# Kernel optimization log

Hardware: AMD Instinct MI355X
Metric: run time of the kernel (lower is better)

Reference implementation:

```python
import jax, jax.numpy as jnp
import numpy as np

B, N, C, D, K, H = 32, 4096, 128, 64, 8, 128  # batch, tokens, in_dim, slot_dim, num_slots, mlp hidden
SCALE = D ** -0.5
EPS = 1e-8
ITERS = 3


def _ln(x, g, b):
    m = jnp.mean(x, axis=-1, keepdims=True)
    v = jnp.var(x, axis=-1, keepdims=True)
    return (x - m) * jax.lax.rsqrt(v + 1e-5) * g + b


def _gru(x, h, wih, whh, bih, bhh):
    # torch.nn.GRUCell semantics; x:[M,D], h:[M,D], wih/whh:[3D,D]
    gi = x @ wih.T + bih
    gh = h @ whh.T + bhh
    i_r, i_z, i_n = jnp.split(gi, 3, axis=-1)
    h_r, h_z, h_n = jnp.split(gh, 3, axis=-1)
    r = jax.nn.sigmoid(i_r + h_r)
    z = jax.nn.sigmoid(i_z + h_z)
    n = jnp.tanh(i_n + r * h_n)
    return (1.0 - z) * n + z * h


def setup_inputs() -> dict:
    key = jax.random.key(0)
    ks = jax.random.split(key, 24)
    f32 = jnp.float32

    def rn(i, shape, scale):
        return (jax.random.normal(ks[i], shape, f32) * scale)

    return {
        "feat": jax.random.normal(ks[0], (B, N, C), f32),
        "slot": jax.random.normal(ks[1], (B, K, D), f32),
        "norm_feat_g": jnp.ones((C,), f32), "norm_feat_b": jnp.zeros((C,), f32),
        "Wk": rn(2, (C, D), C ** -0.5), "Wv": rn(3, (C, D), C ** -0.5),
        "q_ln_g": jnp.ones((D,), f32), "q_ln_b": jnp.zeros((D,), f32),
        "Wq": rn(4, (D, D), D ** -0.5),
        "qbg_ln_g": jnp.ones((D,), f32), "qbg_ln_b": jnp.zeros((D,), f32),
        "Wq_bg": rn(5, (D, D), D ** -0.5),
        "gru_wih": rn(6, (3 * D, D), D ** -0.5), "gru_whh": rn(7, (3 * D, D), D ** -0.5),
        "gru_bih": jnp.zeros((3 * D,), f32), "gru_bhh": jnp.zeros((3 * D,), f32),
        "grubg_wih": rn(8, (3 * D, D), D ** -0.5), "grubg_whh": rn(9, (3 * D, D), D ** -0.5),
        "grubg_bih": jnp.zeros((3 * D,), f32), "grubg_bhh": jnp.zeros((3 * D,), f32),
        "res_ln_g": jnp.ones((D,), f32), "res_ln_b": jnp.zeros((D,), f32),
        "res_w1": rn(10, (D, H), D ** -0.5), "res_b1": jnp.zeros((H,), f32),
        "res_w2": rn(11, (H, D), H ** -0.5), "res_b2": jnp.zeros((D,), f32),
        "resbg_ln_g": jnp.ones((D,), f32), "resbg_ln_b": jnp.zeros((D,), f32),
        "resbg_w1": rn(12, (D, H), D ** -0.5), "resbg_b1": jnp.zeros((H,), f32),
        "resbg_w2": rn(13, (H, D), H ** -0.5), "resbg_b2": jnp.zeros((D,), f32),
    }


def reference(feat, slot, norm_feat_g, norm_feat_b, Wk, Wv,
              q_ln_g, q_ln_b, Wq, qbg_ln_g, qbg_ln_b, Wq_bg,
              gru_wih, gru_whh, gru_bih, gru_bhh,
              grubg_wih, grubg_whh, grubg_bih, grubg_bhh,
              res_ln_g, res_ln_b, res_w1, res_b1, res_w2, res_b2,
              resbg_ln_g, resbg_ln_b, resbg_w1, resbg_b1, resbg_w2, resbg_b2):
    # split externally-provided slots (slot is not None branch)
    slot_bg = slot[:, :1, :]   # [B,1,D]   (bg_slot_dim == fg_slot_dim == D)
    slot_fg = slot[:, 1:, :]   # [B,K-1,D]

    x = _ln(feat, norm_feat_g, norm_feat_b)   # [B,N,C]
    k = x @ Wk                                 # [B,N,D]
    v = x @ Wv                                 # [B,N,D]

    attn = None
    for _ in range(ITERS):
        q_fg = _ln(slot_fg, q_ln_g, q_ln_b) @ Wq          # [B,K-1,D]
        q_bg = _ln(slot_bg, qbg_ln_g, qbg_ln_b) @ Wq_bg   # [B,1,D]
        dots_fg = jnp.einsum('bid,bjd->bij', q_fg, k) * SCALE
        dots_bg = jnp.einsum('bid,bjd->bij', q_bg, k) * SCALE
        dots = jnp.concatenate([dots_bg, dots_fg], axis=1)  # [B,K,N]
        attn = jax.nn.softmax(dots, axis=1) + EPS            # softmax over slots
        attn_bg, attn_fg = attn[:, :1, :], attn[:, 1:, :]
        w_bg = attn_bg / jnp.sum(attn_bg, axis=-1, keepdims=True)
        w_fg = attn_fg / jnp.sum(attn_fg, axis=-1, keepdims=True)
        upd_fg = jnp.einsum('bjd,bij->bid', v, w_fg)  # [B,K-1,D]
        upd_bg = jnp.einsum('bjd,bij->bid', v, w_bg)  # [B,1,D]

        s_bg = _gru(upd_bg.reshape(-1, D), slot_bg.reshape(-1, D),
                    grubg_wih, grubg_whh, grubg_bih, grubg_bhh).reshape(B, 1, D)
        slot_bg = s_bg + (jax.nn.relu(_ln(s_bg, resbg_ln_g, resbg_ln_b) @ resbg_w1 + resbg_b1) @ resbg_w2 + resbg_b2)

        s_fg = _gru(upd_fg.reshape(-1, D), slot_fg.reshape(-1, D),
                    gru_wih, gru_whh, gru_bih, gru_bhh).reshape(B, K - 1, D)
        slot_fg = s_fg + (jax.nn.relu(_ln(s_fg, res_ln_g, res_ln_b) @ res_w1 + res_b1) @ res_w2 + res_b2)

    slots = jnp.concatenate([slot_bg, slot_fg], axis=1)  # [B,K,D]
    return slots, attn
```

## Files before the change

### kernel.cpp

```cpp
#include <hip/hip_runtime.h>
#include <hip/hip_bf16.h>

constexpr int BB = 32;
constexpr int NN = 4096;
constexpr int CC = 128;
constexpr int DD = 64;
constexpr int KK = 8;
constexpr int HH = 128;
constexpr float SCALE = 0.125f;
constexpr float EPS_A = 1e-8f;
constexpr float LN_EPS = 1e-5f;

constexpr int NTIL = 64;

typedef __bf16 bfx8 __attribute__((ext_vector_type(8)));
typedef float f32x4 __attribute__((ext_vector_type(4)));

__device__ inline float wave_sum(float x) {
#pragma unroll
    for (int off = 32; off > 0; off >>= 1) x += __shfl_xor(x, off, 64);
    return x;
}

__device__ inline float lane_bcast(float v, int src) {
    return __uint_as_float(__builtin_amdgcn_readlane(__float_as_uint(v), src));
}

__device__ inline float sigmoidf_(float x) { return 1.f / (1.f + __expf(-x)); }

__device__ inline unsigned short bf16rne(float x) {
    unsigned u = __float_as_uint(x);
    unsigned r = u + 0x7fffu + ((u >> 16) & 1u);
    return (unsigned short)(r >> 16);
}
__device__ inline float bf16tof(unsigned short h) {
    return __uint_as_float(((unsigned)h) << 16);
}

__global__ __launch_bounds__(256) void k0_prepw(
    const float* __restrict__ Wk, const float* __restrict__ Wv,
    unsigned short* __restrict__ fragW)
{
    const int o = blockIdx.x * 256 + threadIdx.x;
    const int j = o & 7, l = (o >> 3) & 63, nf = (o >> 9) & 7, ks = o >> 12;
    const int c = ks * 32 + ((l >> 4) << 3) + j;
    const int n = nf * 16 + (l & 15);
    const float w = (n < DD) ? Wk[c * DD + n] : Wv[c * DD + (n - DD)];
    fragW[o] = bf16rne(w);
}

__global__ __launch_bounds__(256) void k0_prepg(
    const float* __restrict__ fg_ih, const float* __restrict__ fg_hh,
    const float* __restrict__ bg_ih, const float* __restrict__ bg_hh,
    float* __restrict__ wT)
{
    const int o = blockIdx.x * 256 + threadIdx.x;
    const int m = o / (DD * 3 * DD);
    const int rem = o % (DD * 3 * DD);
    const int d = rem / (3 * DD), j = rem % (3 * DD);
    const float* W = (m == 0) ? fg_ih : (m == 1) ? fg_hh : (m == 2) ? bg_ih : bg_hh;
    wT[o] = W[j * DD + d];
}

__global__ __launch_bounds__(256, 4) void k1_mfma(
    const float* __restrict__ feat, const float* __restrict__ nf_g,
    const float* __restrict__ nf_b, const unsigned short* __restrict__ fragW,
    float* __restrict__ kT, float* __restrict__ vout)
{
    __shared__ char ubuf[32768];

    const int tid = threadIdx.x, w = tid >> 6, lane = tid & 63;
    const size_t row0 = (size_t)blockIdx.x * 64;

    const float2 g2 = *(const float2*)&nf_g[2 * lane];
    const float2 b2 = *(const float2*)&nf_b[2 * lane];

#pragma unroll 4
    for (int r0 = 0; r0 < 16; r0++) {
        const int r = w * 16 + r0;
        const float2 x2 = *(const float2*)&feat[(row0 + r) * CC + 2 * lane];
        const float m = wave_sum(x2.x + x2.y) * (1.f / 128.f);
        const float d0 = x2.x - m, d1 = x2.y - m;
        const float var = wave_sum(d0 * d0 + d1 * d1) * (1.f / 128.f);
        const float rs = rsqrtf(var + LN_EPS);
        const float y0 = d0 * rs * g2.x + b2.x;
        const float y1 = d1 * rs * g2.y + b2.y;
        const unsigned short h0 = bf16rne(y0), h1 = bf16rne(y1);
        const unsigned short l0 = bf16rne(y0 - bf16tof(h0));
        const unsigned short l1 = bf16rne(y1 - bf16tof(h1));
        const int off = r * 256 + ((4 * lane) ^ ((r & 7) << 4));
        *(unsigned*)(ubuf + off) = (unsigned)h0 | ((unsigned)h1 << 16);
        *(unsigned*)(ubuf + 16384 + off) = (unsigned)l0 | ((unsigned)l1 << 16);
    }
    __syncthreads();

    f32x4 acc[8];
#pragma unroll
    for (int nf = 0; nf < 8; nf++) acc[nf] = (f32x4){0.f, 0.f, 0.f, 0.f};

    const int arow = w * 16 + (lane & 15);
    const int hi16 = lane >> 4;
    const int asw = (arow & 7) << 4;
#pragma unroll
    for (int ks = 0; ks < 4; ks++) {
        const int abyte = arow * 256 + ((ks * 64 + hi16 * 16) ^ asw);
        const bfx8 ah = __builtin_bit_cast(bfx8, *(const uint4*)(ubuf + abyte));
        const bfx8 al = __builtin_bit_cast(bfx8, *(const uint4*)(ubuf + 16384 + abyte));
#pragma unroll
        for (int nf = 0; nf < 8; nf++) {
            const bfx8 bw = __builtin_bit_cast(
                bfx8, *(const uint4*)(fragW + ((ks * 8 + nf) * 64 + lane) * 8));
            acc[nf] = __builtin_amdgcn_mfma_f32_16x16x32_bf16(ah, bw, acc[nf], 0, 0, 0);
            acc[nf] = __builtin_amdgcn_mfma_f32_16x16x32_bf16(al, bw, acc[nf], 0, 0, 0);
        }
    }
    __syncthreads();

    float* kslds = (float*)ubuf;
    const int trow = w * 16 + (lane >> 4) * 4;
#pragma unroll
    for (int nf = 0; nf < 4; nf++) {
        const int d = nf * 16 + (lane & 15);
#pragma unroll
        for (int reg = 0; reg < 4; reg++)
            kslds[d * 65 + trow + reg] = acc[nf][reg];
    }
    {
        const size_t vbase = (row0 + trow) * DD + (lane & 15);
#pragma unroll
        for (int nf = 4; nf < 8; nf++) {
#pragma unroll
            for (int reg = 0; reg < 4; reg++)
                vout[vbase + (size_t)reg * DD + (nf - 4) * 16] = acc[nf][reg];
        }
    }
    __syncthreads();

    const int b = (int)(row0 >> 12);
    const int n0 = (int)(row0 & 4095);
#pragma unroll
    for (int t = 0; t < 16; t++) {
        const int idx = t * 256 + tid;
        const int d = idx >> 6, nn = idx & 63;
        kT[((size_t)b * DD + d) * NN + n0 + nn] = kslds[d * 65 + nn];
    }
}

__global__ __launch_bounds__(64) void k2_attn(
    const float* __restrict__ kT, const float* __restrict__ v,
    const float* __restrict__ q, float* __restrict__ Upart,
    float* __restrict__ Spart, float* __restrict__ attn_out)
{
    const int blk = blockIdx.x;
    const int b = blk >> 6, tile = blk & 63;
    const int lane = threadIdx.x;
    const int n = (tile << 6) + lane;

    float qreg[KK];
#pragma unroll
    for (int i = 0; i < KK; i++) qreg[i] = q[((size_t)b * KK + i) * DD + lane];

    const float* kp = kT + (size_t)b * DD * NN + n;
    float kv[DD];
#pragma unroll
    for (int d = 0; d < DD; d++) kv[d] = kp[(size_t)d * NN];

    float dots[KK];
#pragma unroll
    for (int i = 0; i < KK; i++) dots[i] = 0.f;
#pragma unroll
    for (int d = 0; d < DD; d++) {
        const float k_ = kv[d];
#pragma unroll
        for (int i = 0; i < KK; i++)
            dots[i] += k_ * lane_bcast(qreg[i], d);
    }
    float m = -1e30f;
#pragma unroll
    for (int i = 0; i < KK; i++) { dots[i] *= SCALE; m = fmaxf(m, dots[i]); }
    float s = 0.f, e[KK];
#pragma unroll
    for (int i = 0; i < KK; i++) { e[i] = __expf(dots[i] - m); s += e[i]; }
    const float inv = 1.f / s;
    float a[KK], sv[KK];
#pragma unroll
    for (int i = 0; i < KK; i++) { a[i] = e[i] * inv + EPS_A; sv[i] = a[i]; }

    if (attn_out) {
#pragma unroll
        for (int i = 0; i < KK; i++)
            attn_out[((size_t)b * KK + i) * NN + n] = a[i];
    }
#pragma unroll
    for (int off = 32; off > 0; off >>= 1) {
#pragma unroll
        for (int i = 0; i < KK; i++) sv[i] += __shfl_xor(sv[i], off, 64);
    }
    if (lane < KK) Spart[(size_t)blk * KK + lane] = sv[lane];

    const float* vp = v + ((size_t)b * NN + (tile << 6)) * DD + lane;
    float vv[64];
#pragma unroll
    for (int t = 0; t < 64; t++) vv[t] = vp[t * DD];

    float U[KK];
#pragma unroll
    for (int i = 0; i < KK; i++) U[i] = 0.f;
#pragma unroll
    for (int t = 0; t < 64; t++) {
        const float vx = vv[t];
#pragma unroll
        for (int i = 0; i < KK; i++)
            U[i] += lane_bcast(a[i], t) * vx;
    }
#pragma unroll
    for (int i = 0; i < KK; i++)
        Upart[((size_t)blk * KK + i) * DD + lane] = U[i];
}

__global__ __launch_bounds__(384) void k3_update(
    const float* __restrict__ Upart, const float* __restrict__ Spart,
    const float* __restrict__ h_in, float* __restrict__ slots_cur,
    float* __restrict__ qout, const float* __restrict__ wT,
    const float* __restrict__ gru_bih, const float* __restrict__ gru_bhh,
    const float* __restrict__ gbg_bih, const float* __restrict__ gbg_bhh,
    const float* __restrict__ res_g, const float* __restrict__ res_b,
    const float* __restrict__ res_w1, const float* __restrict__ res_b1,
    const float* __restrict__ res_w2, const float* __restrict__ res_b2,
    const float* __restrict__ rbg_g, const float* __restrict__ rbg_b,
    const float* __restrict__ rbg_w1, const float* __restrict__ rbg_b1,
    const float* __restrict__ rbg_w2, const float* __restrict__ rbg_b2,
    const float* __restrict__ qln_g, const float* __restrict__ qln_b,
    const float* __restrict__ Wq, const float* __restrict__ qbg_g,
    const float* __restrict__ qbg_b, const float* __restrict__ Wqbg,
    float* __restrict__ out_slots, int do_update)
{
    const int blk = blockIdx.x;
    const int b = blk >> 3, i = blk & 7;
    const int t = threadIdx.x;
    const int fg = (i != 0);

    __shared__ float h_s[DD], upd_s[DD], red[4][DD],
        gih_s[3 * DD], ghh_s[3 * DD], lnx_s[DD], h1_s[HH];

    if (t < DD) h_s[t] = h_in[(size_t)blk * DD + t];

    float sp = 0.f;
    if (do_update) {
        if (t < 256) {
            const int d = t & 63, g = t >> 6;
            float sacc = 0.f;
#pragma unroll
            for (int p = 0; p < 16; p++)
                sacc += Upart[((size_t)(b * NTIL + g * 16 + p) * KK + i) * DD + d];
            red[g][d] = sacc;
        }
        if (t < 64) {
            sp = Spart[(size_t)(b * NTIL + t) * KK + i];
            sp = wave_sum(sp);
        }
        __syncthreads();
        if (t < 64)
            upd_s[t] = (red[0][t] + red[1][t] + red[2][t] + red[3][t]) / sp;
        __syncthreads();

        {
            const int isIH = (t < 3 * DD);
            const int j = isIH ? t : t - 3 * DD;
            const float* w = wT + (size_t)((fg ? 0 : 2) + (isIH ? 0 : 1)) * (DD * 3 * DD);
            const float* xs = isIH ? upd_s : h_s;
            const float* bias = isIH ? (fg ? gru_bih : gbg_bih)
                                     : (fg ? gru_bhh : gbg_bhh);
            float acc = bias[j];
#pragma unroll
            for (int d4 = 0; d4 < 16; d4++) {
                const float4 xv = *(const float4*)&xs[d4 * 4];
                acc += xv.x * w[(d4 * 4 + 0) * 192 + j];
                acc += xv.y * w[(d4 * 4 + 1) * 192 + j];
                acc += xv.z * w[(d4 * 4 + 2) * 192 + j];
                acc += xv.w * w[(d4 * 4 + 3) * 192 + j];
            }
            if (isIH) gih_s[j] = acc; else ghh_s[j] = acc;
        }
        __syncthreads();
    }

    float tmpv = 0.f, newh = 0.f;
    if (do_update) {
        if (t < 64) {
            const float r = sigmoidf_(gih_s[t] + ghh_s[t]);
            const float z = sigmoidf_(gih_s[DD + t] + ghh_s[DD + t]);
            const float ng = tanhf(gih_s[2 * DD + t] + r * ghh_s[2 * DD + t]);
            tmpv = (1.f - z) * ng + z * h_s[t];
            const float m = wave_sum(tmpv) * (1.f / DD);
            const float dv = tmpv - m;
            const float var = wave_sum(dv * dv) * (1.f / DD);
            lnx_s[t] = dv * rsqrtf(var + LN_EPS) * (fg ? res_g : rbg_g)[t] +
                       (fg ? res_b : rbg_b)[t];
        }
        __syncthreads();
        if (t < HH) {
            const float* w1 = fg ? res_w1 : rbg_w1;
            float acc = (fg ? res_b1 : rbg_b1)[t];
#pragma unroll
            for (int d4 = 0; d4 < 16; d4++) {
                const float4 xv = *(const float4*)&lnx_s[d4 * 4];
                acc += xv.x * w1[(d4 * 4 + 0) * HH + t];
                acc += xv.y * w1[(d4 * 4 + 1) * HH + t];
                acc += xv.z * w1[(d4 * 4 + 2) * HH + t];
                acc += xv.w * w1[(d4 * 4 + 3) * HH + t];
            }
            h1_s[t] = fmaxf(acc, 0.f);
        }
        __syncthreads();
        if (t < 64) {
            const float* w2 = fg ? res_w2 : rbg_w2;
            float o = (fg ? res_b2 : rbg_b2)[t];
#pragma unroll
            for (int j4 = 0; j4 < 32; j4++) {
                const float4 hv = *(const float4*)&h1_s[j4 * 4];
                o += hv.x * w2[(j4 * 4 + 0) * DD + t];
                o += hv.y * w2[(j4 * 4 + 1) * DD + t];
                o += hv.z * w2[(j4 * 4 + 2) * DD + t];
                o += hv.w * w2[(j4 * 4 + 3) * DD + t];
            }
            newh = tmpv + o;
        }
    } else {
        if (t < 64) newh = h_s[t];
    }

    if (t < 64) {
        slots_cur[(size_t)blk * DD + t] = newh;
        if (out_slots) out_slots[(size_t)blk * DD + t] = newh;

        const float m2 = wave_sum(newh) * (1.f / DD);
        const float d2 = newh - m2;
        const float v2 = wave_sum(d2 * d2) * (1.f / DD);
        lnx_s[t] = d2 * rsqrtf(v2 + LN_EPS) * (fg ? qln_g : qbg_g)[t] +
                   (fg ? qln_b : qbg_b)[t];
        __builtin_amdgcn_s_waitcnt(0);
        const float* W = fg ? Wq : Wqbg;
        float qv = 0.f;
#pragma unroll
        for (int e4 = 0; e4 < 16; e4++) {
            const float4 xv = *(const float4*)&lnx_s[e4 * 4];
            qv += xv.x * W[(e4 * 4 + 0) * DD + t];
            qv += xv.y * W[(e4 * 4 + 1) * DD + t];
            qv += xv.z * W[(e4 * 4 + 2) * DD + t];
            qv += xv.w * W[(e4 * 4 + 3) * DD + t];
        }
        qout[(size_t)blk * DD + t] = qv;
    }
}

extern "C" void kernel_launch(void* const* d_in, const int* in_sizes, int n_in,
                              void* d_out, int out_size, void* d_ws, size_t ws_size,
                              hipStream_t stream)
{
    const float* feat    = (const float*)d_in[0];
    const float* slot_in = (const float*)d_in[1];
    const float* nf_g    = (const float*)d_in[2];
    const float* nf_b    = (const float*)d_in[3];
    const float* Wk      = (const float*)d_in[4];
    const float* Wv      = (const float*)d_in[5];
    const float* qln_g   = (const float*)d_in[6];
    const float* qln_b   = (const float*)d_in[7];
    const float* Wq      = (const float*)d_in[8];
    const float* qbg_g   = (const float*)d_in[9];
    const float* qbg_b   = (const float*)d_in[10];
    const float* Wqbg    = (const float*)d_in[11];
    const float* gru_wih = (const float*)d_in[12];
    const float* gru_whh = (const float*)d_in[13];
    const float* gru_bih = (const float*)d_in[14];
    const float* gru_bhh = (const float*)d_in[15];
    const float* gbg_wih = (const float*)d_in[16];
    const float* gbg_whh = (const float*)d_in[17];
    const float* gbg_bih = (const float*)d_in[18];
    const float* gbg_bhh = (const float*)d_in[19];
    const float* res_g   = (const float*)d_in[20];
    const float* res_b   = (const float*)d_in[21];
    const float* res_w1  = (const float*)d_in[22];
    const float* res_b1  = (const float*)d_in[23];
    const float* res_w2  = (const float*)d_in[24];
    const float* res_b2  = (const float*)d_in[25];
    const float* rbg_g   = (const float*)d_in[26];
    const float* rbg_b   = (const float*)d_in[27];
    const float* rbg_w1  = (const float*)d_in[28];
    const float* rbg_b1  = (const float*)d_in[29];
    const float* rbg_w2  = (const float*)d_in[30];
    const float* rbg_b2  = (const float*)d_in[31];

    float* out = (float*)d_out;
    char* ws = (char*)d_ws;
    size_t off = 0;
    unsigned short* fragW = (unsigned short*)(ws + off); off += 16384 * 2;
    off = (off + 255) & ~(size_t)255;
    float* wT    = (float*)(ws + off); off += 4 * DD * 3 * DD * 4;
    float* kT    = (float*)(ws + off); off += (size_t)BB * DD * NN * 4;
    float* v     = (float*)(ws + off); off += (size_t)BB * NN * DD * 4;
    float* q     = (float*)(ws + off); off += (size_t)BB * KK * DD * 4;
    float* slots = (float*)(ws + off); off += (size_t)BB * KK * DD * 4;
    float* Upart = (float*)(ws + off); off += (size_t)BB * NTIL * KK * DD * 4;
    float* Spart = (float*)(ws + off); off += (size_t)BB * NTIL * KK * 4;
    if (off > ws_size) return;

    float* out_slots = out;
    float* out_attn  = out + BB * KK * DD;

    k0_prepw<<<64, 256, 0, stream>>>(Wk, Wv, fragW);
    k0_prepg<<<192, 256, 0, stream>>>(gru_wih, gru_whh, gbg_wih, gbg_whh, wT);

    k3_update<<<BB * KK, 384, 0, stream>>>(
        Upart, Spart, slot_in, slots, q, wT,
        gru_bih, gru_bhh, gbg_bih, gbg_bhh,
        res_g, res_b, res_w1, res_b1, res_w2, res_b2,
        rbg_g, rbg_b, rbg_w1, rbg_b1, rbg_w2, rbg_b2,
        qln_g, qln_b, Wq, qbg_g, qbg_b, Wqbg, nullptr, 0);

    k1_mfma<<<BB * NN / 64, 256, 0, stream>>>(feat, nf_g, nf_b, fragW, kT, v);

    for (int it = 0; it < 3; it++) {
        k2_attn<<<BB * NTIL, 64, 0, stream>>>(
            kT, v, q, Upart, Spart, it == 2 ? out_attn : nullptr);
        k3_update<<<BB * KK, 384, 0, stream>>>(
            Upart, Spart, slots, slots, q, wT,
            gru_bih, gru_bhh, gbg_bih, gbg_bhh,
            res_g, res_b, res_w1, res_b1, res_w2, res_b2,
            rbg_g, rbg_b, rbg_w1, rbg_b1, rbg_w2, rbg_b2,
            qln_g, qln_b, Wq, qbg_g, qbg_b, Wqbg,
            it == 2 ? out_slots : nullptr, 1);
    }
}
```

Measured before the change: 268.2 us.

## Fuse all stages into one cooperative persistent kernel with grid syncs

Replaces the chain of prep, projection, attention and slot-update launches with a single cooperative persistent kernel that loops over tiles and tasks and separates phases with grid-wide syncs. The slot update is rewritten as a one-wave-per-slot routine using lane broadcasts instead of a 384-thread block with shared memory. The aim is to remove per-launch overhead and the idle tails between the nine dependent launches. In exchange, the projection phase is capped at 512 resident blocks, which may reduce overlap, and each grid sync plus the small slot-update phase leaves most of the GPU idle.

```diff
diff --git a/kernel.cpp b/kernel.cpp
--- a/kernel.cpp
+++ b/kernel.cpp
@@ -1,5 +1,8 @@
 #include <hip/hip_runtime.h>
+#include <hip/hip_cooperative_groups.h>
 #include <hip/hip_bf16.h>
+
+namespace cg = cooperative_groups;
 
 constexpr int BB = 32;
 constexpr int NN = 4096;
@@ -12,6 +15,7 @@
 constexpr float LN_EPS = 1e-5f;
 
 constexpr int NTIL = 64;
+constexpr int NCU  = 256;
 
 typedef __bf16 bfx8 __attribute__((ext_vector_type(8)));
 typedef float f32x4 __attribute__((ext_vector_type(4)));
@@ -35,6 +39,286 @@
 }
 __device__ inline float bf16tof(unsigned short h) {
     return __uint_as_float(((unsigned)h) << 16);
+}
+
+struct MegaArgs {
+    const float *feat, *slot_in, *nf_g, *nf_b, *Wk, *Wv;
+    const float *qln_g, *qln_b, *Wq, *qbg_g, *qbg_b, *Wqbg;
+    const float *gru_wih, *gru_whh, *gru_bih, *gru_bhh;
+    const float *gbg_wih, *gbg_whh, *gbg_bih, *gbg_bhh;
+    const float *res_g, *res_b, *res_w1, *res_b1, *res_w2, *res_b2;
+    const float *rbg_g, *rbg_b, *rbg_w1, *rbg_b1, *rbg_w2, *rbg_b2;
+    unsigned short *fragW;
+    float *wT, *kT, *v, *q, *slots, *Upart, *Spart;
+    float *out_slots, *out_attn;
+};
+
+__device__ __forceinline__ void slot_update_wave(
+    const MegaArgs& A, int b, int i, int lane, bool init, bool last)
+{
+    const int fg = (i != 0);
+    const size_t slot_off = ((size_t)b * KK + i) * DD + lane;
+    const float h = init ? A.slot_in[slot_off] : A.slots[slot_off];
+    float newh = h;
+
+    if (!init) {
+        float sp = A.Spart[((size_t)b * NTIL + lane) * KK + i];
+        sp = wave_sum(sp);
+        float us = 0.f;
+#pragma unroll 8
+        for (int p = 0; p < NTIL; p++)
+            us += A.Upart[(((size_t)b * NTIL + p) * KK + i) * DD + lane];
+        const float upd = us / sp;
+
+        const float* wih = A.wT + (size_t)(fg ? 0 : 2) * (DD * 3 * DD);
+        const float* whh = wih + DD * 3 * DD;
+        const float* bih = fg ? A.gru_bih : A.gbg_bih;
+        const float* bhh = fg ? A.gru_bhh : A.gbg_bhh;
+        float gi0 = bih[lane], gi1 = bih[DD + lane], gi2 = bih[2 * DD + lane];
+        float gh0 = bhh[lane], gh1 = bhh[DD + lane], gh2 = bhh[2 * DD + lane];
+#pragma unroll 4
+        for (int d = 0; d < DD; d++) {
+            const float ud = lane_bcast(upd, d);
+            const float hd = lane_bcast(h, d);
+            gi0 += ud * wih[d * 192 + lane];
+            gi1 += ud * wih[d * 192 + DD + lane];
+            gi2 += ud * wih[d * 192 + 2 * DD + lane];
+            gh0 += hd * whh[d * 192 + lane];
+            gh1 += hd * whh[d * 192 + DD + lane];
+            gh2 += hd * whh[d * 192 + 2 * DD + lane];
+        }
+        const float r = sigmoidf_(gi0 + gh0);
+        const float z = sigmoidf_(gi1 + gh1);
+        const float ng = tanhf(gi2 + r * gh2);
+        const float tmp = (1.f - z) * ng + z * h;
+
+        const float m = wave_sum(tmp) * (1.f / DD);
+        const float dv = tmp - m;
+        const float var = wave_sum(dv * dv) * (1.f / DD);
+        const float lnx = dv * rsqrtf(var + LN_EPS) * (fg ? A.res_g : A.rbg_g)[lane] +
+                          (fg ? A.res_b : A.rbg_b)[lane];
+        const float* w1 = fg ? A.res_w1 : A.rbg_w1;
+        const float* b1 = fg ? A.res_b1 : A.rbg_b1;
+        float a0 = b1[lane], a1 = b1[DD + lane];
+#pragma unroll 4
+        for (int d = 0; d < DD; d++) {
+            const float xd = lane_bcast(lnx, d);
+            a0 += xd * w1[d * HH + lane];
+            a1 += xd * w1[d * HH + DD + lane];
+        }
+        a0 = fmaxf(a0, 0.f); a1 = fmaxf(a1, 0.f);
+        const float* w2 = fg ? A.res_w2 : A.rbg_w2;
+        float o = (fg ? A.res_b2 : A.rbg_b2)[lane];
+#pragma unroll 4
+        for (int j = 0; j < DD; j++)
+            o += lane_bcast(a0, j) * w2[j * DD + lane];
+#pragma unroll 4
+        for (int j = 0; j < DD; j++)
+            o += lane_bcast(a1, j) * w2[(DD + j) * DD + lane];
+        newh = tmp + o;
+    }
+
+    A.slots[slot_off] = newh;
+    if (last) A.out_slots[slot_off] = newh;
+
+    const float m2 = wave_sum(newh) * (1.f / DD);
+    const float d2 = newh - m2;
+    const float v2 = wave_sum(d2 * d2) * (1.f / DD);
+    const float lq = d2 * rsqrtf(v2 + LN_EPS) * (fg ? A.qln_g : A.qbg_g)[lane] +
+                     (fg ? A.qln_b : A.qbg_b)[lane];
+    const float* W = fg ? A.Wq : A.Wqbg;
+    float qv = 0.f;
+#pragma unroll 4
+    for (int e = 0; e < DD; e++)
+        qv += lane_bcast(lq, e) * W[e * DD + lane];
+    A.q[slot_off] = qv;
+}
+
+__global__ __launch_bounds__(256, 2) void mega(MegaArgs A)
+{
+    cg::grid_group grid = cg::this_grid();
+    __shared__ char ubuf[32768];
+
+    const int tid = threadIdx.x, w = tid >> 6, lane = tid & 63;
+    const int G = gridDim.x;
+
+    for (int o = blockIdx.x * 256 + tid; o < 16384; o += G * 256) {
+        const int j = o & 7, l = (o >> 3) & 63, nf = (o >> 9) & 7, ks = o >> 12;
+        const int c = ks * 32 + ((l >> 4) << 3) + j;
+        const int n = nf * 16 + (l & 15);
+        const float wv = (n < DD) ? A.Wk[c * DD + n] : A.Wv[c * DD + (n - DD)];
+        A.fragW[o] = bf16rne(wv);
+    }
+    for (int o = blockIdx.x * 256 + tid; o < 4 * DD * 3 * DD; o += G * 256) {
+        const int m = o / (DD * 3 * DD);
+        const int rem = o % (DD * 3 * DD);
+        const int d = rem / (3 * DD), j = rem % (3 * DD);
+        const float* W = (m == 0) ? A.gru_wih : (m == 1) ? A.gru_whh
+                       : (m == 2) ? A.gbg_wih : A.gbg_whh;
+        A.wT[o] = W[j * DD + d];
+    }
+    for (int task = blockIdx.x * 4 + w; task < BB * KK; task += G * 4)
+        slot_update_wave(A, task >> 3, task & 7, lane, true, false);
+    __threadfence();
+    grid.sync();
+
+    for (int tile = blockIdx.x; tile < BB * NN / 64; tile += G) {
+        __syncthreads();
+        const size_t row0 = (size_t)tile * 64;
+
+        const float2 g2 = *(const float2*)&A.nf_g[2 * lane];
+        const float2 b2 = *(const float2*)&A.nf_b[2 * lane];
+#pragma unroll 4
+        for (int r0 = 0; r0 < 16; r0++) {
+            const int r = w * 16 + r0;
+            const float2 x2 = *(const float2*)&A.feat[(row0 + r) * CC + 2 * lane];
+            const float m = wave_sum(x2.x + x2.y) * (1.f / 128.f);
+            const float d0 = x2.x - m, d1 = x2.y - m;
+            const float var = wave_sum(d0 * d0 + d1 * d1) * (1.f / 128.f);
+            const float rs = rsqrtf(var + LN_EPS);
+            const float y0 = d0 * rs * g2.x + b2.x;
+            const float y1 = d1 * rs * g2.y + b2.y;
+            const unsigned short h0 = bf16rne(y0), h1 = bf16rne(y1);
+            const unsigned short l0 = bf16rne(y0 - bf16tof(h0));
+            const unsigned short l1 = bf16rne(y1 - bf16tof(h1));
+            const int off = r * 256 + ((4 * lane) ^ ((r & 7) << 4));
+            *(unsigned*)(ubuf + off) = (unsigned)h0 | ((unsigned)h1 << 16);
+            *(unsigned*)(ubuf + 16384 + off) = (unsigned)l0 | ((unsigned)l1 << 16);
+        }
+        __syncthreads();
+
+        f32x4 acc[8];
+#pragma unroll
+        for (int nf = 0; nf < 8; nf++) acc[nf] = (f32x4){0.f, 0.f, 0.f, 0.f};
+        const int arow = w * 16 + (lane & 15);
+        const int hi16 = lane >> 4;
+        const int asw = (arow & 7) << 4;
+#pragma unroll
+        for (int ks = 0; ks < 4; ks++) {
+            const int abyte = arow * 256 + ((ks * 64 + hi16 * 16) ^ asw);
+            const bfx8 ah = __builtin_bit_cast(bfx8, *(const uint4*)(ubuf + abyte));
+            const bfx8 al = __builtin_bit_cast(bfx8, *(const uint4*)(ubuf + 16384 + abyte));
+#pragma unroll
+            for (int nf = 0; nf < 8; nf++) {
+                const bfx8 bw = __builtin_bit_cast(
+                    bfx8, *(const uint4*)(A.fragW + ((ks * 8 + nf) * 64 + lane) * 8));
+                acc[nf] = __builtin_amdgcn_mfma_f32_16x16x32_bf16(ah, bw, acc[nf], 0, 0, 0);
+                acc[nf] = __builtin_amdgcn_mfma_f32_16x16x32_bf16(al, bw, acc[nf], 0, 0, 0);
+            }
+        }
+        __syncthreads();
+
+        float* kslds = (float*)ubuf;
+        const int trow = w * 16 + (lane >> 4) * 4;
+#pragma unroll
+        for (int nf = 0; nf < 4; nf++) {
+            const int d = nf * 16 + (lane & 15);
+#pragma unroll
+            for (int reg = 0; reg < 4; reg++)
+                kslds[d * 65 + trow + reg] = acc[nf][reg];
+        }
+        {
+            const size_t vbase = (row0 + trow) * DD + (lane & 15);
+#pragma unroll
+            for (int nf = 4; nf < 8; nf++) {
+#pragma unroll
+                for (int reg = 0; reg < 4; reg++)
+                    A.v[vbase + (size_t)reg * DD + (nf - 4) * 16] = acc[nf][reg];
+            }
+        }
+        __syncthreads();
+
+        const int b = (int)(row0 >> 12);
+        const int n0 = (int)(row0 & 4095);
+#pragma unroll
+        for (int t = 0; t < 16; t++) {
+            const int idx = t * 256 + tid;
+            const int d = idx >> 6, nn = idx & 63;
+            A.kT[((size_t)b * DD + d) * NN + n0 + nn] = kslds[d * 65 + nn];
+        }
+    }
+    __threadfence();
+    grid.sync();
+
+    for (int it = 0; it < 3; it++) {
+        for (int task = blockIdx.x * 4 + w; task < BB * NTIL; task += G * 4) {
+            const int b = task >> 6, tile = task & 63;
+            const int n = (tile << 6) + lane;
+
+            float qreg[KK];
+#pragma unroll
+            for (int i = 0; i < KK; i++)
+                qreg[i] = A.q[((size_t)b * KK + i) * DD + lane];
+
+            const float* kp = A.kT + (size_t)b * DD * NN + n;
+            float kv[DD];
+#pragma unroll
+            for (int d = 0; d < DD; d++) kv[d] = kp[(size_t)d * NN];
+
+            float dots[KK];
+#pragma unroll
+            for (int i = 0; i < KK; i++) dots[i] = 0.f;
+#pragma unroll
+            for (int d = 0; d < DD; d++) {
+                const float k_ = kv[d];
+#pragma unroll
+                for (int i = 0; i < KK; i++)
+                    dots[i] += k_ * lane_bcast(qreg[i], d);
+            }
+            float mx = -1e30f;
+#pragma unroll
+            for (int i = 0; i < KK; i++) { dots[i] *= SCALE; mx = fmaxf(mx, dots[i]); }
+            float s = 0.f, e[KK];
+#pragma unroll
+            for (int i = 0; i < KK; i++) { e[i] = __expf(dots[i] - mx); s += e[i]; }
+            const float inv = 1.f / s;
+            float a[KK], sv[KK];
+#pragma unroll
+            for (int i = 0; i < KK; i++) { a[i] = e[i] * inv + EPS_A; sv[i] = a[i]; }
+
+            if (it == 2) {
+#pragma unroll
+                for (int i = 0; i < KK; i++)
+                    A.out_attn[((size_t)b * KK + i) * NN + n] = a[i];
+            }
+#pragma unroll
+            for (int off = 32; off > 0; off >>= 1) {
+#pragma unroll
+                for (int i = 0; i < KK; i++) sv[i] += __shfl_xor(sv[i], off, 64);
+            }
+            if (lane == 0) {
+#pragma unroll
+                for (int i = 0; i < KK; i++)
+                    A.Spart[(size_t)task * KK + i] = sv[i];
+            }
+
+            const float* vp = A.v + ((size_t)b * NN + (tile << 6)) * DD + lane;
+            float vv[64];
+#pragma unroll
+            for (int t = 0; t < 64; t++) vv[t] = vp[t * DD];
+
+            float U[KK];
+#pragma unroll
+            for (int i = 0; i < KK; i++) U[i] = 0.f;
+#pragma unroll
+            for (int t = 0; t < 64; t++) {
+                const float vx = vv[t];
+#pragma unroll
+                for (int i = 0; i < KK; i++)
+                    U[i] += lane_bcast(a[i], t) * vx;
+            }
+#pragma unroll
+            for (int i = 0; i < KK; i++)
+                A.Upart[((size_t)task * KK + i) * DD + lane] = U[i];
+        }
+        __threadfence();
+        grid.sync();
+
+        for (int task = blockIdx.x * 4 + w; task < BB * KK; task += G * 4)
+            slot_update_wave(A, task >> 3, task & 7, lane, false, it == 2);
+        __threadfence();
+        grid.sync();
+    }
 }
 
 __global__ __launch_bounds__(256) void k0_prepw(
@@ -68,13 +352,10 @@
     float* __restrict__ kT, float* __restrict__ vout)
 {
     __shared__ char ubuf[32768];
-
     const int tid = threadIdx.x, w = tid >> 6, lane = tid & 63;
     const size_t row0 = (size_t)blockIdx.x * 64;
-
     const float2 g2 = *(const float2*)&nf_g[2 * lane];
     const float2 b2 = *(const float2*)&nf_b[2 * lane];
-
 #pragma unroll 4
     for (int r0 = 0; r0 < 16; r0++) {
         const int r = w * 16 + r0;
@@ -93,11 +374,9 @@
         *(unsigned*)(ubuf + 16384 + off) = (unsigned)l0 | ((unsigned)l1 << 16);
     }
     __syncthreads();
-
     f32x4 acc[8];
 #pragma unroll
     for (int nf = 0; nf < 8; nf++) acc[nf] = (f32x4){0.f, 0.f, 0.f, 0.f};
-
     const int arow = w * 16 + (lane & 15);
     const int hi16 = lane >> 4;
     const int asw = (arow & 7) << 4;
@@ -115,7 +394,6 @@
         }
     }
     __syncthreads();
-
     float* kslds = (float*)ubuf;
     const int trow = w * 16 + (lane >> 4) * 4;
 #pragma unroll
@@ -135,7 +413,6 @@
         }
     }
     __syncthreads();
-
     const int b = (int)(row0 >> 12);
     const int n0 = (int)(row0 & 4095);
 #pragma unroll
@@ -196,7 +473,10 @@
 #pragma unroll
         for (int i = 0; i < KK; i++) sv[i] += __shfl_xor(sv[i], off, 64);
     }
-    if (lane < KK) Spart[(size_t)blk * KK + lane] = sv[lane];
+    if (lane == 0) {
+#pragma unroll
+        for (int i = 0; i < KK; i++) Spart[(size_t)blk * KK + i] = sv[i];
+    }
 
     const float* vp = v + ((size_t)b * NN + (tile << 6)) * DD + lane;
     float vv[64];
@@ -218,217 +498,88 @@
         Upart[((size_t)blk * KK + i) * DD + lane] = U[i];
 }
 
-__global__ __launch_bounds__(384) void k3_update(
-    const float* __restrict__ Upart, const float* __restrict__ Spart,
-    const float* __restrict__ h_in, float* __restrict__ slots_cur,
-    float* __restrict__ qout, const float* __restrict__ wT,
-    const float* __restrict__ gru_bih, const float* __restrict__ gru_bhh,
-    const float* __restrict__ gbg_bih, const float* __restrict__ gbg_bhh,
-    const float* __restrict__ res_g, const float* __restrict__ res_b,
-    const float* __restrict__ res_w1, const float* __restrict__ res_b1,
-    const float* __restrict__ res_w2, const float* __restrict__ res_b2,
-    const float* __restrict__ rbg_g, const float* __restrict__ rbg_b,
-    const float* __restrict__ rbg_w1, const float* __restrict__ rbg_b1,
-    const float* __restrict__ rbg_w2, const float* __restrict__ rbg_b2,
-    const float* __restrict__ qln_g, const float* __restrict__ qln_b,
-    const float* __restrict__ Wq, const float* __restrict__ qbg_g,
-    const float* __restrict__ qbg_b, const float* __restrict__ Wqbg,
-    float* __restrict__ out_slots, int do_update)
-{
-    const int blk = blockIdx.x;
-    const int b = blk >> 3, i = blk & 7;
-    const int t = threadIdx.x;
-    const int fg = (i != 0);
-
-    __shared__ float h_s[DD], upd_s[DD], red[4][DD],
-        gih_s[3 * DD], ghh_s[3 * DD], lnx_s[DD], h1_s[HH];
-
-    if (t < DD) h_s[t] = h_in[(size_t)blk * DD + t];
-
-    float sp = 0.f;
-    if (do_update) {
-        if (t < 256) {
-            const int d = t & 63, g = t >> 6;
-            float sacc = 0.f;
-#pragma unroll
-            for (int p = 0; p < 16; p++)
-                sacc += Upart[((size_t)(b * NTIL + g * 16 + p) * KK + i) * DD + d];
-            red[g][d] = sacc;
-        }
-        if (t < 64) {
-            sp = Spart[(size_t)(b * NTIL + t) * KK + i];
-            sp = wave_sum(sp);
-        }
-        __syncthreads();
-        if (t < 64)
-            upd_s[t] = (red[0][t] + red[1][t] + red[2][t] + red[3][t]) / sp;
-        __syncthreads();
-
-        {
-            const int isIH = (t < 3 * DD);
-            const int j = isIH ? t : t - 3 * DD;
-            const float* w = wT + (size_t)((fg ? 0 : 2) + (isIH ? 0 : 1)) * (DD * 3 * DD);
-            const float* xs = isIH ? upd_s : h_s;
-            const float* bias = isIH ? (fg ? gru_bih : gbg_bih)
-                                     : (fg ? gru_bhh : gbg_bhh);
-            float acc = bias[j];
-#pragma unroll
-            for (int d4 = 0; d4 < 16; d4++) {
-                const float4 xv = *(const float4*)&xs[d4 * 4];
-                acc += xv.x * w[(d4 * 4 + 0) * 192 + j];
-                acc += xv.y * w[(d4 * 4 + 1) * 192 + j];
-                acc += xv.z * w[(d4 * 4 + 2) * 192 + j];
-                acc += xv.w * w[(d4 * 4 + 3) * 192 + j];
-            }
-            if (isIH) gih_s[j] = acc; else ghh_s[j] = acc;
-        }
-        __syncthreads();
-    }
-
-    float tmpv = 0.f, newh = 0.f;
-    if (do_update) {
-        if (t < 64) {
-            const float r = sigmoidf_(gih_s[t] + ghh_s[t]);
-            const float z = sigmoidf_(gih_s[DD + t] + ghh_s[DD + t]);
-            const float ng = tanhf(gih_s[2 * DD + t] + r * ghh_s[2 * DD + t]);
-            tmpv = (1.f - z) * ng + z * h_s[t];
-            const float m = wave_sum(tmpv) * (1.f / DD);
-            const float dv = tmpv - m;
-            const float var = wave_sum(dv * dv) * (1.f / DD);
-            lnx_s[t] = dv * rsqrtf(var + LN_EPS) * (fg ? res_g : rbg_g)[t] +
-                       (fg ? res_b : rbg_b)[t];
-        }
-        __syncthreads();
-        if (t < HH) {
-            const float* w1 = fg ? res_w1 : rbg_w1;
-            float acc = (fg ? res_b1 : rbg_b1)[t];
-#pragma unroll
-            for (int d4 = 0; d4 < 16; d4++) {
-                const float4 xv = *(const float4*)&lnx_s[d4 * 4];
-                acc += xv.x * w1[(d4 * 4 + 0) * HH + t];
-                acc += xv.y * w1[(d4 * 4 + 1) * HH + t];
-                acc += xv.z * w1[(d4 * 4 + 2) * HH + t];
-                acc += xv.w * w1[(d4 * 4 + 3) * HH + t];
-            }
-            h1_s[t] = fmaxf(acc, 0.f);
-        }
-        __syncthreads();
-        if (t < 64) {
-            const float* w2 = fg ? res_w2 : rbg_w2;
-            float o = (fg ? res_b2 : rbg_b2)[t];
-#pragma unroll
-            for (int j4 = 0; j4 < 32; j4++) {
-                const float4 hv = *(const float4*)&h1_s[j4 * 4];
-                o += hv.x * w2[(j4 * 4 + 0) * DD + t];
-                o += hv.y * w2[(j4 * 4 + 1) * DD + t];
-                o += hv.z * w2[(j4 * 4 + 2) * DD + t];
-                o += hv.w * w2[(j4 * 4 + 3) * DD + t];
-            }
-            newh = tmpv + o;
-        }
-    } else {
-        if (t < 64) newh = h_s[t];
-    }
-
-    if (t < 64) {
-        slots_cur[(size_t)blk * DD + t] = newh;
-        if (out_slots) out_slots[(size_t)blk * DD + t] = newh;
-
-        const float m2 = wave_sum(newh) * (1.f / DD);
-        const float d2 = newh - m2;
-        const float v2 = wave_sum(d2 * d2) * (1.f / DD);
-        lnx_s[t] = d2 * rsqrtf(v2 + LN_EPS) * (fg ? qln_g : qbg_g)[t] +
-                   (fg ? qln_b : qbg_b)[t];
-        __builtin_amdgcn_s_waitcnt(0);
-        const float* W = fg ? Wq : Wqbg;
-        float qv = 0.f;
-#pragma unroll
-        for (int e4 = 0; e4 < 16; e4++) {
-            const float4 xv = *(const float4*)&lnx_s[e4 * 4];
-            qv += xv.x * W[(e4 * 4 + 0) * DD + t];
-            qv += xv.y * W[(e4 * 4 + 1) * DD + t];
-            qv += xv.z * W[(e4 * 4 + 2) * DD + t];
-            qv += xv.w * W[(e4 * 4 + 3) * DD + t];
-        }
-        qout[(size_t)blk * DD + t] = qv;
-    }
+__global__ __launch_bounds__(64) void k3_update(MegaArgs A, int it)
+{
+    const int task = blockIdx.x;
+    slot_update_wave(A, task >> 3, task & 7, (int)threadIdx.x,
+                     it < 0, it == 2);
 }
 
 extern "C" void kernel_launch(void* const* d_in, const int* in_sizes, int n_in,
                               void* d_out, int out_size, void* d_ws, size_t ws_size,
                               hipStream_t stream)
 {
-    const float* feat    = (const float*)d_in[0];
-    const float* slot_in = (const float*)d_in[1];
-    const float* nf_g    = (const float*)d_in[2];
-    const float* nf_b    = (const float*)d_in[3];
-    const float* Wk      = (const float*)d_in[4];
-    const float* Wv      = (const float*)d_in[5];
-    const float* qln_g   = (const float*)d_in[6];
-    const float* qln_b   = (const float*)d_in[7];
-    const float* Wq      = (const float*)d_in[8];
-    const float* qbg_g   = (const float*)d_in[9];
-    const float* qbg_b   = (const float*)d_in[10];
-    const float* Wqbg    = (const float*)d_in[11];
-    const float* gru_wih = (const float*)d_in[12];
-    const float* gru_whh = (const float*)d_in[13];
-    const float* gru_bih = (const float*)d_in[14];
-    const float* gru_bhh = (const float*)d_in[15];
-    const float* gbg_wih = (const float*)d_in[16];
-    const float* gbg_whh = (const float*)d_in[17];
-    const float* gbg_bih = (const float*)d_in[18];
-    const float* gbg_bhh = (const float*)d_in[19];
-    const float* res_g   = (const float*)d_in[20];
-    const float* res_b   = (const float*)d_in[21];
-    const float* res_w1  = (const float*)d_in[22];
-    const float* res_b1  = (const float*)d_in[23];
-    const float* res_w2  = (const float*)d_in[24];
-    const float* res_b2  = (const float*)d_in[25];
-    const float* rbg_g   = (const float*)d_in[26];
-    const float* rbg_b   = (const float*)d_in[27];
-    const float* rbg_w1  = (const float*)d_in[28];
-    const float* rbg_b1  = (const float*)d_in[29];
-    const float* rbg_w2  = (const float*)d_in[30];
-    const float* rbg_b2  = (const float*)d_in[31];
-
-    float* out = (float*)d_out;
+    MegaArgs a;
+    a.feat    = (const float*)d_in[0];
+    a.slot_in = (const float*)d_in[1];
+    a.nf_g    = (const float*)d_in[2];
+    a.nf_b    = (const float*)d_in[3];
+    a.Wk      = (const float*)d_in[4];
+    a.Wv      = (const float*)d_in[5];
+    a.qln_g   = (const float*)d_in[6];
+    a.qln_b   = (const float*)d_in[7];
+    a.Wq      = (const float*)d_in[8];
+    a.qbg_g   = (const float*)d_in[9];
+    a.qbg_b   = (const float*)d_in[10];
+    a.Wqbg    = (const float*)d_in[11];
+    a.gru_wih = (const float*)d_in[12];
+    a.gru_whh = (const float*)d_in[13];
+    a.gru_bih = (const float*)d_in[14];
+    a.gru_bhh = (const float*)d_in[15];
+    a.gbg_wih = (const float*)d_in[16];
+    a.gbg_whh = (const float*)d_in[17];
+    a.gbg_bih = (const float*)d_in[18];
+    a.gbg_bhh = (const float*)d_in[19];
+    a.res_g   = (const float*)d_in[20];
+    a.res_b   = (const float*)d_in[21];
+    a.res_w1  = (const float*)d_in[22];
+    a.res_b1  = (const float*)d_in[23];
+    a.res_w2  = (const float*)d_in[24];
+    a.res_b2  = (const float*)d_in[25];
+    a.rbg_g   = (const float*)d_in[26];
+    a.rbg_b   = (const float*)d_in[27];
+    a.rbg_w1  = (const float*)d_in[28];
+    a.rbg_b1  = (const float*)d_in[29];
+    a.rbg_w2  = (const float*)d_in[30];
+    a.rbg_b2  = (const float*)d_in[31];
+
     char* ws = (char*)d_ws;
     size_t off = 0;
-    unsigned short* fragW = (unsigned short*)(ws + off); off += 16384 * 2;
+    a.fragW = (unsigned short*)(ws + off); off += 16384 * 2;
     off = (off + 255) & ~(size_t)255;
-    float* wT    = (float*)(ws + off); off += 4 * DD * 3 * DD * 4;
-    float* kT    = (float*)(ws + off); off += (size_t)BB * DD * NN * 4;
-    float* v     = (float*)(ws + off); off += (size_t)BB * NN * DD * 4;
-    float* q     = (float*)(ws + off); off += (size_t)BB * KK * DD * 4;
-    float* slots = (float*)(ws + off); off += (size_t)BB * KK * DD * 4;
-    float* Upart = (float*)(ws + off); off += (size_t)BB * NTIL * KK * DD * 4;
-    float* Spart = (float*)(ws + off); off += (size_t)BB * NTIL * KK * 4;
+    a.wT    = (float*)(ws + off); off += 4 * DD * 3 * DD * 4;
+    a.kT    = (float*)(ws + off); off += (size_t)BB * DD * NN * 4;
+    a.v     = (float*)(ws + off); off += (size_t)BB * NN * DD * 4;
+    a.q     = (float*)(ws + off); off += (size_t)BB * KK * DD * 4;
+    a.slots = (float*)(ws + off); off += (size_t)BB * KK * DD * 4;
+    a.Upart = (float*)(ws + off); off += (size_t)BB * NTIL * KK * DD * 4;
+    a.Spart = (float*)(ws + off); off += (size_t)BB * NTIL * KK * 4;
     if (off > ws_size) return;
 
-    float* out_slots = out;
-    float* out_attn  = out + BB * KK * DD;
-
-    k0_prepw<<<64, 256, 0, stream>>>(Wk, Wv, fragW);
-    k0_prepg<<<192, 256, 0, stream>>>(gru_wih, gru_whh, gbg_wih, gbg_whh, wT);
-
-    k3_update<<<BB * KK, 384, 0, stream>>>(
-        Upart, Spart, slot_in, slots, q, wT,
-        gru_bih, gru_bhh, gbg_bih, gbg_bhh,
-        res_g, res_b, res_w1, res_b1, res_w2, res_b2,
-        rbg_g, rbg_b, rbg_w1, rbg_b1, rbg_w2, rbg_b2,
-        qln_g, qln_b, Wq, qbg_g, qbg_b, Wqbg, nullptr, 0);
-
-    k1_mfma<<<BB * NN / 64, 256, 0, stream>>>(feat, nf_g, nf_b, fragW, kT, v);
-
+    a.out_slots = (float*)d_out;
+    a.out_attn  = (float*)d_out + BB * KK * DD;
+
+    hipError_t lerr = hipErrorUnknown;
+    int maxb = 0;
+    if (hipOccupancyMaxActiveBlocksPerMultiprocessor(
+            &maxb, reinterpret_cast<const void*>(mega), 256, 0) == hipSuccess &&
+        maxb > 0) {
+        int grid = maxb * NCU;
+        if (grid > 512) grid = 512;
+        void* kargs[] = { &a };
+        lerr = hipLaunchCooperativeKernel(reinterpret_cast<void*>(mega),
+                                          dim3(grid), dim3(256), kargs, 0, stream);
+    }
+    if (lerr == hipSuccess) return;
+    (void)hipGetLastError();
+
+    k0_prepw<<<64, 256, 0, stream>>>(a.Wk, a.Wv, a.fragW);
+    k0_prepg<<<192, 256, 0, stream>>>(a.gru_wih, a.gru_whh, a.gbg_wih, a.gbg_whh, a.wT);
+    k3_update<<<BB * KK, 64, 0, stream>>>(a, -1);
+    k1_mfma<<<BB * NN / 64, 256, 0, stream>>>(a.feat, a.nf_g, a.nf_b, a.fragW, a.kT, a.v);
     for (int it = 0; it < 3; it++) {
         k2_attn<<<BB * NTIL, 64, 0, stream>>>(
-            kT, v, q, Upart, Spart, it == 2 ? out_attn : nullptr);
-        k3_update<<<BB * KK, 384, 0, stream>>>(
-            Upart, Spart, slots, slots, q, wT,
-            gru_bih, gru_bhh, gbg_bih, gbg_bhh,
-            res_g, res_b, res_w1, res_b1, res_w2, res_b2,
-            rbg_g, rbg_b, rbg_w1, rbg_b1, rbg_w2, rbg_b2,
-            qln_g, qln_b, Wq, qbg_g, qbg_b, Wqbg,
-            it == 2 ? out_slots : nullptr, 1);
-    }
-}
+            a.kT, a.v, a.q, a.Upart, a.Spart, it == 2 ? a.out_attn : nullptr);
+        k3_update<<<BB * KK, 64, 0, stream>>>(a, it);
+    }
+}
```

After: 827.6 us. 3.09x slower.
